# Kernel optimization log

Measured on AMD Instinct MI355X. Metric: run time of the kernel, lower is better.

Reference implementation:

```python
import jax, jax.numpy as jnp
import numpy as np
from jax.ops import segment_sum, segment_max

N, F, H, HEADS, E, OUT = 50000, 256, 64, 4, 800000, 16


def setup_inputs() -> dict:
    key = jax.random.key(0)
    ks = jax.random.split(key, 16)
    s = 0.05
    return {
        "x": jax.random.normal(ks[0], (N, F), jnp.float32),
        "edge_index": jax.random.randint(ks[1], (2, E), 0, N, jnp.int64),
        # GCN layer params
        "W_gcn1": jax.random.normal(ks[2], (F, H), jnp.float32) * s,
        "b_gcn1": jnp.zeros((H,), jnp.float32),
        "W_gcn2": jax.random.normal(ks[3], (H, OUT), jnp.float32) * s,
        "b_gcn2": jnp.zeros((OUT,), jnp.float32),
        # GAT layer 1 (heads=HEADS, concat)
        "W_gat1": jax.random.normal(ks[4], (F, HEADS * H), jnp.float32) * s,
        "a_src1": jax.random.normal(ks[5], (HEADS, H), jnp.float32) * s,
        "a_dst1": jax.random.normal(ks[6], (HEADS, H), jnp.float32) * s,
        "b_gat1": jnp.zeros((HEADS * H,), jnp.float32),
        # GAT layer 2 (heads=1, concat=False)
        "W_gat2": jax.random.normal(ks[7], (HEADS * H, OUT), jnp.float32) * s,
        "a_src2": jax.random.normal(ks[8], (1, OUT), jnp.float32) * s,
        "a_dst2": jax.random.normal(ks[9], (1, OUT), jnp.float32) * s,
        "b_gat2": jnp.zeros((OUT,), jnp.float32),
    }


def _add_self_loops(edge_index, n):
    loop = jnp.arange(n, dtype=edge_index.dtype)
    src = jnp.concatenate([edge_index[0], loop])
    dst = jnp.concatenate([edge_index[1], loop])
    return src, dst


def _gcn(x, src, dst, norm, W, b, n):
    h = x @ W  # [N, out]
    out = segment_sum(h[src] * norm[:, None], dst, num_segments=n)
    return out + b


def _gat(x, src, dst, W, a_s, a_d, b, heads, concat, n):
    h = (x @ W).reshape(n, heads, -1)  # [N, heads, C]
    s_src = jnp.einsum("nhc,hc->nh", h, a_s)
    s_dst = jnp.einsum("nhc,hc->nh", h, a_d)
    e = jax.nn.leaky_relu(s_src[src] + s_dst[dst], 0.2)  # [Etot, heads]
    m = segment_max(e, dst, num_segments=n)               # per-dst softmax
    p = jnp.exp(e - m[dst])
    denom = segment_sum(p, dst, num_segments=n)
    alpha = p / denom[dst]
    out = segment_sum(h[src] * alpha[..., None], dst, num_segments=n)
    out = out.reshape(n, -1) if concat else out.mean(axis=1)
    return out + b


def reference(x, edge_index, W_gcn1, b_gcn1, W_gcn2, b_gcn2,
              W_gat1, a_src1, a_dst1, b_gat1,
              W_gat2, a_src2, a_dst2, b_gat2):
    n = x.shape[0]
    src, dst = _add_self_loops(edge_index, n)
    # symmetric GCN normalization on self-loop-augmented graph
    deg = segment_sum(jnp.ones_like(dst, x.dtype), dst, num_segments=n)
    dinv = jnp.where(deg > 0, jax.lax.rsqrt(deg), 0.0)
    norm = dinv[src] * dinv[dst]

    x_gcn = jax.nn.relu(_gcn(x, src, dst, norm, W_gcn1, b_gcn1, n))
    x_gcn = _gcn(x_gcn, src, dst, norm, W_gcn2, b_gcn2, n)

    x_gat = jax.nn.relu(_gat(x, src, dst, W_gat1, a_src1, a_dst1, b_gat1, HEADS, True, n))
    x_gat = _gat(x_gat, src, dst, W_gat2, a_src2, a_dst2, b_gat2, 1, False, n)

    return jnp.concatenate([x_gcn, x_gat], axis=1)
```

## Files before the change

### kernel.cpp

```cpp
#include <hip/hip_runtime.h>
#include <math.h>

#define NN     50000
#define FF     256
#define HH     64
#define NHEADS 4
#define EE     800000
#define OUTD   16

typedef __attribute__((ext_vector_type(8))) short short8;
typedef __attribute__((ext_vector_type(4))) float f32x4;

__device__ inline unsigned short f2bf(float f) {
    unsigned u = __builtin_bit_cast(unsigned, f);
    unsigned r = (u + 0x7fff + ((u >> 16) & 1)) >> 16;
    return (unsigned short)r;
}
__device__ inline float bf2f(unsigned short s) {
    unsigned u = ((unsigned)s) << 16;
    return __builtin_bit_cast(float, u);
}

__global__ void k_zero_int(int* __restrict__ p, int n) {
    int i = blockIdx.x * blockDim.x + threadIdx.x;
    if (i < n) p[i] = 0;
}

__global__ void k_count(const int* __restrict__ dst, int* __restrict__ cnt, int e) {
    int i = blockIdx.x * blockDim.x + threadIdx.x;
    if (i < e) atomicAdd(&cnt[dst[i]], 1);
}

__global__ __launch_bounds__(256) void k_scan_a(const int* __restrict__ cnt,
                                                int* __restrict__ partial, int n) {
    int i = blockIdx.x * 256 + threadIdx.x;
    int v = (i < n) ? cnt[i] : 0;
#pragma unroll
    for (int off = 32; off >= 1; off >>= 1) v += __shfl_xor(v, off, 64);
    __shared__ int ws[4];
    int wave = threadIdx.x >> 6;
    if ((threadIdx.x & 63) == 0) ws[wave] = v;
    __syncthreads();
    if (threadIdx.x == 0) partial[blockIdx.x] = ws[0] + ws[1] + ws[2] + ws[3];
}

__global__ __launch_bounds__(256) void k_scan_b(const int* __restrict__ partial,
                                                int* __restrict__ blockoff,
                                                int* __restrict__ total_out, int nb) {
    __shared__ int arr[256];
    int tid = threadIdx.x;
    arr[tid] = (tid < nb) ? partial[tid] : 0;
    __syncthreads();
#pragma unroll
    for (int off = 1; off < 256; off <<= 1) {
        int v = arr[tid];
        int add = (tid >= off) ? arr[tid - off] : 0;
        __syncthreads();
        arr[tid] = v + add;
        __syncthreads();
    }
    if (tid < nb) blockoff[tid] = arr[tid] - partial[tid];
    if (tid == 0) *total_out = arr[255];
}

__global__ __launch_bounds__(256) void k_scan_c(const int* __restrict__ cnt,
                                                const int* __restrict__ blockoff,
                                                int* __restrict__ row_start,
                                                int* __restrict__ cursor,
                                                float* __restrict__ dinv, int n) {
    __shared__ int arr[256];
    int tid = threadIdx.x;
    int i = blockIdx.x * 256 + tid;
    int c = (i < n) ? cnt[i] : 0;
    arr[tid] = c;
    __syncthreads();
#pragma unroll
    for (int off = 1; off < 256; off <<= 1) {
        int v = arr[tid];
        int add = (tid >= off) ? arr[tid - off] : 0;
        __syncthreads();
        arr[tid] = v + add;
        __syncthreads();
    }
    if (i < n) {
        int excl = arr[tid] - c + blockoff[blockIdx.x];
        row_start[i] = excl;
        cursor[i] = excl;
        dinv[i] = rsqrtf((float)(c + 1));
    }
}

__global__ void k_fill(const int* __restrict__ src, const int* __restrict__ dst,
                       int* __restrict__ cursor, int* __restrict__ col, int e) {
    int i = blockIdx.x * blockDim.x + threadIdx.x;
    if (i < e) {
        int d = dst[i];
        int pos = atomicAdd(&cursor[d], 1);
        col[pos] = src[i];
    }
}

__device__ inline void pack_one(const float* __restrict__ W,
                                unsigned short* __restrict__ bhi,
                                unsigned short* __restrict__ blo,
                                int t_, int NT, int NTOT, int TOFF, int SRC_NC) {
    int lane = t_ & 63;
    int tile = (t_ >> 6) % NT;
    int kb = (t_ >> 6) / NT;
    int q = lane >> 4, c = lane & 15;
    size_t off = ((size_t)(kb * NTOT + TOFF + tile) * 64 + lane) * 8;
#pragma unroll
    for (int j = 0; j < 8; j++) {
        float w = W[(size_t)(kb * 32 + q * 8 + j) * SRC_NC + tile * 16 + c];
        unsigned short h = f2bf(w);
        bhi[off + j] = h;
        if (blo) blo[off + j] = f2bf(w - bf2f(h));
    }
}

#define NTT 20
__global__ __launch_bounds__(256) void k_pack_all(const float* __restrict__ Wg1,
                                                  const float* __restrict__ Wgat1,
                                                  const float* __restrict__ Wg2,
                                                  const float* __restrict__ Wgat2,
                                                  unsigned short* __restrict__ bhiC,
                                                  unsigned short* __restrict__ bhiG2,
                                                  unsigned short* __restrict__ bloG2,
                                                  unsigned short* __restrict__ bhiA2,
                                                  unsigned short* __restrict__ bloA2) {
    int t = blockIdx.x * 256 + threadIdx.x;
    if (t < 2048)        pack_one(Wg1,   bhiC,  nullptr, t,         4,  NTT, 0, 64);
    else if (t < 10240)  pack_one(Wgat1, bhiC,  nullptr, t - 2048,  16, NTT, 4, 256);
    else if (t < 10368)  pack_one(Wg2,   bhiG2, bloG2,   t - 10240, 1,  1,   0, 16);
    else if (t < 10880)  pack_one(Wgat2, bhiA2, bloA2,   t - 10368, 1,  1,   0, 16);
}

__global__ __launch_bounds__(256) void mfma_gemm_fused(const float* __restrict__ A,
                                                       const unsigned short* __restrict__ Bhi,
                                                       unsigned short* __restrict__ Ch1,
                                                       unsigned short* __restrict__ Chg,
                                                       const float* __restrict__ dinv,
                                                       const float* __restrict__ a_s,
                                                       const float* __restrict__ a_d,
                                                       float* __restrict__ ssrc,
                                                       float* __restrict__ sdst,
                                                       int M) {
    const int K = 256;
    __shared__ short8 bsh[NTT * 64];
    int tid = threadIdx.x;
    int w = tid >> 6, lane = tid & 63, q = lane >> 4, c = lane & 15;
    int row_base = blockIdx.x * 64 + w * 16;
    int ar = min(row_base + c, M - 1);
    const float* ap = A + (size_t)ar * K + q * 8;

    f32x4 acc[NTT];
#pragma unroll
    for (int t = 0; t < NTT; t++) acc[t] = (f32x4){0.f, 0.f, 0.f, 0.f};

    for (int kb = 0; kb < 8; kb++) {
        float av[8];
        *(float4*)(av)     = *(const float4*)(ap + kb * 32);
        *(float4*)(av + 4) = *(const float4*)(ap + kb * 32 + 4);
        short8 ahi, alo;
#pragma unroll
        for (int j = 0; j < 8; j++) {
            unsigned short h = f2bf(av[j]);
            ahi[j] = (short)h;
            alo[j] = (short)f2bf(av[j] - bf2f(h));
        }
        const short8* gh = (const short8*)(Bhi + (size_t)kb * NTT * 512);
        __syncthreads();
        for (int i = tid; i < NTT * 64; i += 256) bsh[i] = gh[i];
        __syncthreads();
#pragma unroll
        for (int t = 0; t < NTT; t++) {
            short8 bhi = bsh[t * 64 + lane];
            acc[t] = __builtin_amdgcn_mfma_f32_16x16x32_bf16(ahi, bhi, acc[t], 0, 0, 0);
            acc[t] = __builtin_amdgcn_mfma_f32_16x16x32_bf16(alo, bhi, acc[t], 0, 0, 0);
        }
    }

#pragma unroll
    for (int i = 0; i < 4; i++) {
        int r = row_base + q * 4 + i;
        float ss[4] = {0.f, 0.f, 0.f, 0.f};
        float sd[4] = {0.f, 0.f, 0.f, 0.f};
#pragma unroll
        for (int t = 0; t < 16; t++) {
            float v = acc[t + 4][i];
            ss[t >> 2] += v * a_s[t * 16 + c];
            sd[t >> 2] += v * a_d[t * 16 + c];
        }
#pragma unroll
        for (int h = 0; h < 4; h++) {
#pragma unroll
            for (int off = 1; off <= 8; off <<= 1) {
                ss[h] += __shfl_xor(ss[h], off, 16);
                sd[h] += __shfl_xor(sd[h], off, 16);
            }
        }
        if (c == i && r < M) {
            *(float4*)(ssrc + (size_t)r * 4) = make_float4(ss[0], ss[1], ss[2], ss[3]);
            *(float4*)(sdst + (size_t)r * 4) = make_float4(sd[0], sd[1], sd[2], sd[3]);
        }
    }

#pragma unroll
    for (int i = 0; i < 4; i++) {
        int r = row_base + q * 4 + i;
        if (r < M) {
            float sc = dinv[r];
#pragma unroll
            for (int t = 0; t < 4; t++)
                Ch1[(size_t)r * 64 + t * 16 + c] = f2bf(acc[t][i] * sc);
#pragma unroll
            for (int t = 0; t < 16; t++)
                Chg[(size_t)r * 256 + t * 16 + c] = f2bf(acc[t + 4][i]);
        }
    }
}

template <int KB, bool SCALE, bool SC2, int OFS>
__global__ __launch_bounds__(256) void mfma_n16(const unsigned short* __restrict__ A,
                                                const unsigned short* __restrict__ Bhi,
                                                const unsigned short* __restrict__ Blo,
                                                unsigned short* __restrict__ Cbf,
                                                const float* __restrict__ rowscale,
                                                const float* __restrict__ a_s2,
                                                const float* __restrict__ a_d2,
                                                float* __restrict__ s2s,
                                                float* __restrict__ s2d, int M) {
    const int K = KB * 32;
    int tid = threadIdx.x;
    int w = tid >> 6, lane = tid & 63, q = lane >> 4, c = lane & 15;
    int row_base = blockIdx.x * 64 + w * 16;
    int ar = min(row_base + c, M - 1);
    const unsigned short* ap = A + (size_t)ar * K + q * 8;
    f32x4 acc = (f32x4){0.f, 0.f, 0.f, 0.f};
#pragma unroll
    for (int kb = 0; kb < KB; kb++) {
        short8 av = *(const short8*)(ap + kb * 32);
        size_t bo = ((size_t)kb * 64 + lane) * 8;
        short8 bh = *(const short8*)(Bhi + bo);
        short8 bl = *(const short8*)(Blo + bo);
        acc = __builtin_amdgcn_mfma_f32_16x16x32_bf16(av, bh, acc, 0, 0, 0);
        acc = __builtin_amdgcn_mfma_f32_16x16x32_bf16(av, bl, acc, 0, 0, 0);
    }
    if (SC2) {
#pragma unroll
        for (int i = 0; i < 4; i++) {
            float ps = acc[i] * a_s2[c];
            float pd = acc[i] * a_d2[c];
#pragma unroll
            for (int off = 1; off <= 8; off <<= 1) {
                ps += __shfl_xor(ps, off, 16);
                pd += __shfl_xor(pd, off, 16);
            }
            int r = row_base + q * 4 + i;
            if (c == i && r < M) {
                s2s[r] = ps;
                s2d[r] = pd;
            }
        }
    }
#pragma unroll
    for (int i = 0; i < 4; i++) {
        int r = row_base + q * 4 + i;
        if (r < M) {
            float sc = SCALE ? rowscale[r] : 1.0f;
            Cbf[((size_t)r * 16 + c) * 2 + OFS] = f2bf(acc[i] * sc);
        }
    }
}

__global__ __launch_bounds__(256) void gcn1_agg(const unsigned short* __restrict__ h,
                                                const int* __restrict__ rs,
                                                const int* __restrict__ col,
                                                const float* __restrict__ dinv,
                                                const float* __restrict__ b,
                                                unsigned short* __restrict__ out) {
    int wid = (blockIdx.x * 256 + threadIdx.x) >> 6;
    int lane = threadIdx.x & 63;
    if (wid >= NN) return;
    int g = lane >> 4;
    int cidx = (lane & 15) * 4;
    float di = dinv[wid];
    int beg = rs[wid], end = rs[wid + 1];
    float4 acc = make_float4(0.f, 0.f, 0.f, 0.f);

    for (int j0 = beg; j0 < end; j0 += 64) {
        int cnt = min(64, end - j0);
        int sreg = 0;
        if (lane < cnt) sreg = col[j0 + lane];
        for (int e = 0; e < cnt; e += 16) {
            int m0 = e + g, m1 = e + g + 4, m2 = e + g + 8, m3 = e + g + 12;
            int s0 = __shfl(sreg, m0, 64);
            int s1 = __shfl(sreg, m1, 64);
            int s2 = __shfl(sreg, m2, 64);
            int s3 = __shfl(sreg, m3, 64);
            ushort4 v0 = make_ushort4(0, 0, 0, 0), v1 = make_ushort4(0, 0, 0, 0);
            ushort4 v2 = make_ushort4(0, 0, 0, 0), v3 = make_ushort4(0, 0, 0, 0);
            if (m0 < cnt) v0 = *(const ushort4*)(h + (size_t)s0 * HH + cidx);
            if (m1 < cnt) v1 = *(const ushort4*)(h + (size_t)s1 * HH + cidx);
            if (m2 < cnt) v2 = *(const ushort4*)(h + (size_t)s2 * HH + cidx);
            if (m3 < cnt) v3 = *(const ushort4*)(h + (size_t)s3 * HH + cidx);
            acc.x += (bf2f(v0.x) + bf2f(v1.x)) + (bf2f(v2.x) + bf2f(v3.x));
            acc.y += (bf2f(v0.y) + bf2f(v1.y)) + (bf2f(v2.y) + bf2f(v3.y));
            acc.z += (bf2f(v0.z) + bf2f(v1.z)) + (bf2f(v2.z) + bf2f(v3.z));
            acc.w += (bf2f(v0.w) + bf2f(v1.w)) + (bf2f(v2.w) + bf2f(v3.w));
        }
    }
#pragma unroll
    for (int off = 16; off <= 32; off <<= 1) {
        acc.x += __shfl_xor(acc.x, off, 64);
        acc.y += __shfl_xor(acc.y, off, 64);
        acc.z += __shfl_xor(acc.z, off, 64);
        acc.w += __shfl_xor(acc.w, off, 64);
    }
    if (g == 0) {
        ushort4 sv = *(const ushort4*)(h + (size_t)wid * HH + cidx);
        float4 bv = *(const float4*)(b + cidx);
        ushort4 o;
        o.x = f2bf(fmaxf((acc.x + bf2f(sv.x)) * di + bv.x, 0.f));
        o.y = f2bf(fmaxf((acc.y + bf2f(sv.y)) * di + bv.y, 0.f));
        o.z = f2bf(fmaxf((acc.z + bf2f(sv.z)) * di + bv.z, 0.f));
        o.w = f2bf(fmaxf((acc.w + bf2f(sv.w)) * di + bv.w, 0.f));
        *(ushort4*)(out + (size_t)wid * HH + cidx) = o;
    }
}

__global__ __launch_bounds__(256) void gat1_agg(const unsigned short* __restrict__ hg,
                                                const int* __restrict__ rs,
                                                const int* __restrict__ col,
                                                const float* __restrict__ ssrc,
                                                const float* __restrict__ sdst,
                                                const float* __restrict__ b,
                                                unsigned short* __restrict__ out) {
    __shared__ int s_lds[4][64];
    __shared__ float p_lds[4][64 * 4];
    int tid = threadIdx.x;
    int w = tid >> 6, lane = tid & 63;
    int wid = blockIdx.x * 4 + w;
    int hh = lane >> 4;
    int* sl = s_lds[w];
    float* pl = p_lds[w];

    float4 sd4 = *(const float4*)(sdst + (size_t)wid * 4);
    float sdv[4] = {sd4.x, sd4.y, sd4.z, sd4.w};
    float4 sf4 = *(const float4*)(ssrc + (size_t)wid * 4);
    float sfv[4] = {sf4.x, sf4.y, sf4.z, sf4.w};
    float psf[4];
#pragma unroll
    for (int h = 0; h < 4; h++) {
        float e = sfv[h] + sdv[h];
        e = (e >= 0.f) ? e : 0.2f * e;
        psf[h] = __expf(e);
    }
    float pse = (hh & 2) ? ((hh & 1) ? psf[3] : psf[2]) : ((hh & 1) ? psf[1] : psf[0]);
    const unsigned short* hbase = hg + lane * 4;
    ushort4 hvs = *(const ushort4*)(hbase + (size_t)wid * 256);
    float4 acc;
    acc.x = bf2f(hvs.x) * pse; acc.y = bf2f(hvs.y) * pse;
    acc.z = bf2f(hvs.z) * pse; acc.w = bf2f(hvs.w) * pse;

    float lsum[4] = {0.f, 0.f, 0.f, 0.f};
    int beg = rs[wid], end = rs[wid + 1];
    for (int j0 = beg; j0 < end; j0 += 64) {
        int cnt = min(64, end - j0);
        if (lane < cnt) {
            int sreg = col[j0 + lane];
            float4 sv = *(const float4*)(ssrc + (size_t)sreg * 4);
            float svv[4] = {sv.x, sv.y, sv.z, sv.w};
            float pv[4];
#pragma unroll
            for (int h = 0; h < 4; h++) {
                float e = svv[h] + sdv[h];
                e = (e >= 0.f) ? e : 0.2f * e;
                pv[h] = __expf(e);
                lsum[h] += pv[h];
            }
            sl[lane] = sreg;
            *(float4*)&pl[lane * 4] = make_float4(pv[0], pv[1], pv[2], pv[3]);
        }
        int e = 0;
        for (; e + 4 <= cnt; e += 4) {
            int s0 = sl[e], s1 = sl[e + 1], s2 = sl[e + 2], s3 = sl[e + 3];
            float p0 = pl[e * 4 + hh], p1 = pl[(e + 1) * 4 + hh];
            float p2 = pl[(e + 2) * 4 + hh], p3 = pl[(e + 3) * 4 + hh];
            ushort4 h0 = *(const ushort4*)(hbase + (size_t)s0 * 256);
            ushort4 h1 = *(const ushort4*)(hbase + (size_t)s1 * 256);
            ushort4 h2 = *(const ushort4*)(hbase + (size_t)s2 * 256);
            ushort4 h3 = *(const ushort4*)(hbase + (size_t)s3 * 256);
            acc.x += bf2f(h0.x) * p0; acc.y += bf2f(h0.y) * p0;
            acc.z += bf2f(h0.z) * p0; acc.w += bf2f(h0.w) * p0;
            acc.x += bf2f(h1.x) * p1; acc.y += bf2f(h1.y) * p1;
            acc.z += bf2f(h1.z) * p1; acc.w += bf2f(h1.w) * p1;
            acc.x += bf2f(h2.x) * p2; acc.y += bf2f(h2.y) * p2;
            acc.z += bf2f(h2.z) * p2; acc.w += bf2f(h2.w) * p2;
            acc.x += bf2f(h3.x) * p3; acc.y += bf2f(h3.y) * p3;
            acc.z += bf2f(h3.z) * p3; acc.w += bf2f(h3.w) * p3;
        }
        for (; e < cnt; e++) {
            int s = sl[e];
            float p = pl[e * 4 + hh];
            ushort4 hv = *(const ushort4*)(hbase + (size_t)s * 256);
            acc.x += bf2f(hv.x) * p; acc.y += bf2f(hv.y) * p;
            acc.z += bf2f(hv.z) * p; acc.w += bf2f(hv.w) * p;
        }
    }
#pragma unroll
    for (int h = 0; h < 4; h++) {
        float v = lsum[h];
        for (int off = 32; off >= 1; off >>= 1) v += __shfl_xor(v, off, 64);
        lsum[h] = v + psf[h];
    }
    float lt = (hh & 2) ? ((hh & 1) ? lsum[3] : lsum[2]) : ((hh & 1) ? lsum[1] : lsum[0]);
    float li = 1.0f / lt;
    float4 bv = *(const float4*)(b + lane * 4);
    ushort4 o;
    o.x = f2bf(fmaxf(acc.x * li + bv.x, 0.f));
    o.y = f2bf(fmaxf(acc.y * li + bv.y, 0.f));
    o.z = f2bf(fmaxf(acc.z * li + bv.z, 0.f));
    o.w = f2bf(fmaxf(acc.w * li + bv.w, 0.f));
    *(ushort4*)(out + (size_t)wid * 256 + lane * 4) = o;
}

__global__ __launch_bounds__(256) void final_agg(const unsigned* __restrict__ hp,
                                                 const int* __restrict__ rs,
                                                 const int* __restrict__ col,
                                                 const float* __restrict__ dinv,
                                                 const float* __restrict__ s2s,
                                                 const float* __restrict__ s2d,
                                                 const float* __restrict__ bg2,
                                                 const float* __restrict__ bga2,
                                                 float* __restrict__ out) {
    int t = blockIdx.x * 256 + threadIdx.x;
    int node = t >> 4;
    int c = t & 15;
    float di = dinv[node];
    float sd = s2d[node];
    float es = s2s[node] + sd;
    es = (es >= 0.f) ? es : 0.2f * es;
    float psf = __expf(es);
    unsigned pvs = hp[(size_t)node * 16 + c];
    float accg = bf2f((unsigned short)pvs);
    float acca = bf2f((unsigned short)(pvs >> 16)) * psf;
    float lp = 0.f;
    int beg = rs[node], end = rs[node + 1];
    for (int j0 = beg; j0 < end; j0 += 16) {
        int cnt = min(16, end - j0);
        int sreg = 0;
        float pr = 0.f;
        if (c < cnt) {
            sreg = col[j0 + c];
            float e = s2s[sreg] + sd;
            e = (e >= 0.f) ? e : 0.2f * e;
            pr = __expf(e);
            lp += pr;
        }
        for (int e = 0; e < cnt; e += 4) {
            int si[4];
            float pi[4];
#pragma unroll
            for (int u = 0; u < 4; u++) {
                si[u] = __shfl(sreg, (e + u) & 15, 16);
                pi[u] = __shfl(pr, (e + u) & 15, 16);
            }
            unsigned hv[4];
#pragma unroll
            for (int u = 0; u < 4; u++) hv[u] = hp[(size_t)si[u] * 16 + c];
#pragma unroll
            for (int u = 0; u < 4; u++) {
                if (e + u < cnt) {
                    accg += bf2f((unsigned short)hv[u]);
                    acca += bf2f((unsigned short)(hv[u] >> 16)) * pi[u];
                }
            }
        }
    }
    for (int off = 8; off >= 1; off >>= 1) lp += __shfl_xor(lp, off, 16);
    float l = lp + psf;
    out[(size_t)node * 32 + c] = accg * di + bg2[c];
    out[(size_t)node * 32 + 16 + c] = acca / l + bga2[c];
}

extern "C" void kernel_launch(void* const* d_in, const int* in_sizes, int n_in,
                              void* d_out, int out_size, void* d_ws, size_t ws_size,
                              hipStream_t stream) {
    const float* x      = (const float*)d_in[0];
    const int*   ei     = (const int*)d_in[1];
    const float* Wg1    = (const float*)d_in[2];
    const float* bg1    = (const float*)d_in[3];
    const float* Wg2    = (const float*)d_in[4];
    const float* bg2    = (const float*)d_in[5];
    const float* Wgat1  = (const float*)d_in[6];
    const float* a_src1 = (const float*)d_in[7];
    const float* a_dst1 = (const float*)d_in[8];
    const float* bgat1  = (const float*)d_in[9];
    const float* Wgat2  = (const float*)d_in[10];
    const float* a_src2 = (const float*)d_in[11];
    const float* a_dst2 = (const float*)d_in[12];
    const float* bgat2  = (const float*)d_in[13];
    float* out = (float*)d_out;

    const int* e_src = ei;
    const int* e_dst = ei + EE;

    char* wsb = (char*)d_ws;
    size_t o = 0;
    auto alloc = [&](size_t bytes) -> void* {
        void* p = wsb + o;
        o += (bytes + 255) & ~(size_t)255;
        return p;
    };
    float* dinv            = (float*)alloc(NN * 4);
    float* ssrc1           = (float*)alloc((size_t)NN * 16);
    float* sdst1           = (float*)alloc((size_t)NN * 16);
    unsigned short* h1b    = (unsigned short*)alloc((size_t)NN * HH * 2);
    unsigned short* xg1    = (unsigned short*)alloc((size_t)NN * HH * 2);
    unsigned short* hgb    = (unsigned short*)alloc((size_t)NN * 256 * 2);
    unsigned short* xgat1  = (unsigned short*)alloc((size_t)NN * 256 * 2);
    unsigned short* pairb  = (unsigned short*)alloc((size_t)NN * 16 * 4);
    float* s2src           = (float*)alloc(NN * 4);
    float* s2dst           = (float*)alloc(NN * 4);
    unsigned short* bhiC   = (unsigned short*)alloc((size_t)8 * NTT * 512 * 2);
    unsigned short* bhiG2  = (unsigned short*)alloc(64 * 16 * 2);
    unsigned short* bloG2  = (unsigned short*)alloc(64 * 16 * 2);
    unsigned short* bhiA2  = (unsigned short*)alloc(256 * 16 * 2);
    unsigned short* bloA2  = (unsigned short*)alloc(256 * 16 * 2);
    int* cnt               = (int*)alloc(NN * 4);
    int* rowstart          = (int*)alloc((NN + 1) * 4);
    int* cursor            = (int*)alloc(NN * 4);
    int* colarr            = (int*)alloc((size_t)EE * 4);
    int* partial           = (int*)alloc(256 * 4);
    int* blockoff          = (int*)alloc(256 * 4);

    const int TB = 256;
    const int NB = (NN + 255) / 256;
    k_zero_int<<<(NN + TB - 1) / TB, TB, 0, stream>>>(cnt, NN);
    k_count<<<(EE + TB - 1) / TB, TB, 0, stream>>>(e_dst, cnt, EE);
    k_scan_a<<<NB, TB, 0, stream>>>(cnt, partial, NN);
    k_scan_b<<<1, TB, 0, stream>>>(partial, blockoff, rowstart + NN, NB);
    k_scan_c<<<NB, TB, 0, stream>>>(cnt, blockoff, rowstart, cursor, dinv, NN);
    k_fill<<<(EE + TB - 1) / TB, TB, 0, stream>>>(e_src, e_dst, cursor, colarr, EE);
    k_pack_all<<<(10880 + TB - 1) / TB, TB, 0, stream>>>(Wg1, Wgat1, Wg2, Wgat2,
                                                         bhiC, bhiG2, bloG2,
                                                         bhiA2, bloA2);

    const int GB = (NN + 63) / 64;
    const int G16 = (NN * 16) / 256;

    mfma_gemm_fused<<<GB, TB, 0, stream>>>(x, bhiC, h1b, hgb, dinv,
                                           a_src1, a_dst1, ssrc1, sdst1, NN);

    gcn1_agg<<<(NN * 64) / TB, TB, 0, stream>>>(h1b, rowstart, colarr, dinv, bg1, xg1);
    mfma_n16<2, true, false, 0><<<GB, TB, 0, stream>>>(xg1, bhiG2, bloG2, pairb, dinv,
                                                       nullptr, nullptr, nullptr, nullptr, NN);

    gat1_agg<<<NN / 4, TB, 0, stream>>>(hgb, rowstart, colarr, ssrc1, sdst1, bgat1, xgat1);
    mfma_n16<8, false, true, 1><<<GB, TB, 0, stream>>>(xgat1, bhiA2, bloA2, pairb, nullptr,
                                                       a_src2, a_dst2, s2src, s2dst, NN);

    final_agg<<<G16, TB, 0, stream>>>((const unsigned*)pairb, rowstart, colarr, dinv,
                                      s2src, s2dst, bg2, bgat2, out);
}
```

Before: 358.1 us.

## Fuse GCN and GAT aggregations, merge second-layer GEMMs, drop LDS staging

Merges the GCN layer-1 aggregation into the GAT layer-1 aggregation kernel so both read the CSR neighbor list once and share the staged source indices. Combines the two small N=16 MFMA GEMMs into one launch by splitting blocks between them. Also removes the LDS staging and barriers for B in the first GEMM, reading B fragments directly from global/cache instead. This cuts kernel launches, repeated index reads and sync overhead, but adds register pressure in the fused aggregation and more global loads of B in the big GEMM.

```diff
diff --git a/kernel.cpp b/kernel.cpp
--- a/kernel.cpp
+++ b/kernel.cpp
@@ -146,12 +146,12 @@
                                                        float* __restrict__ sdst,
                                                        int M) {
     const int K = 256;
-    __shared__ short8 bsh[NTT * 64];
     int tid = threadIdx.x;
     int w = tid >> 6, lane = tid & 63, q = lane >> 4, c = lane & 15;
     int row_base = blockIdx.x * 64 + w * 16;
     int ar = min(row_base + c, M - 1);
     const float* ap = A + (size_t)ar * K + q * 8;
+    const short8* bp = (const short8*)Bhi + lane;
 
     f32x4 acc[NTT];
 #pragma unroll
@@ -168,13 +168,9 @@
             ahi[j] = (short)h;
             alo[j] = (short)f2bf(av[j] - bf2f(h));
         }
-        const short8* gh = (const short8*)(Bhi + (size_t)kb * NTT * 512);
-        __syncthreads();
-        for (int i = tid; i < NTT * 64; i += 256) bsh[i] = gh[i];
-        __syncthreads();
 #pragma unroll
         for (int t = 0; t < NTT; t++) {
-            short8 bhi = bsh[t * 64 + lane];
+            short8 bhi = bp[(size_t)(kb * NTT + t) * 64];
             acc[t] = __builtin_amdgcn_mfma_f32_16x16x32_bf16(ahi, bhi, acc[t], 0, 0, 0);
             acc[t] = __builtin_amdgcn_mfma_f32_16x16x32_bf16(alo, bhi, acc[t], 0, 0, 0);
         }
@@ -221,19 +217,19 @@
 }
 
 template <int KB, bool SCALE, bool SC2, int OFS>
-__global__ __launch_bounds__(256) void mfma_n16(const unsigned short* __restrict__ A,
-                                                const unsigned short* __restrict__ Bhi,
-                                                const unsigned short* __restrict__ Blo,
-                                                unsigned short* __restrict__ Cbf,
-                                                const float* __restrict__ rowscale,
-                                                const float* __restrict__ a_s2,
-                                                const float* __restrict__ a_d2,
-                                                float* __restrict__ s2s,
-                                                float* __restrict__ s2d, int M) {
+__device__ inline void n16_body(int bx, int tid,
+                                const unsigned short* __restrict__ A,
+                                const unsigned short* __restrict__ Bhi,
+                                const unsigned short* __restrict__ Blo,
+                                unsigned short* __restrict__ Cbf,
+                                const float* __restrict__ rowscale,
+                                const float* __restrict__ a_s2,
+                                const float* __restrict__ a_d2,
+                                float* __restrict__ s2s,
+                                float* __restrict__ s2d, int M) {
     const int K = KB * 32;
-    int tid = threadIdx.x;
     int w = tid >> 6, lane = tid & 63, q = lane >> 4, c = lane & 15;
-    int row_base = blockIdx.x * 64 + w * 16;
+    int row_base = bx * 64 + w * 16;
     int ar = min(row_base + c, M - 1);
     const unsigned short* ap = A + (size_t)ar * K + q * 8;
     f32x4 acc = (f32x4){0.f, 0.f, 0.f, 0.f};
@@ -273,78 +269,50 @@
     }
 }
 
-__global__ __launch_bounds__(256) void gcn1_agg(const unsigned short* __restrict__ h,
-                                                const int* __restrict__ rs,
-                                                const int* __restrict__ col,
-                                                const float* __restrict__ dinv,
-                                                const float* __restrict__ b,
-                                                unsigned short* __restrict__ out) {
-    int wid = (blockIdx.x * 256 + threadIdx.x) >> 6;
-    int lane = threadIdx.x & 63;
-    if (wid >= NN) return;
-    int g = lane >> 4;
-    int cidx = (lane & 15) * 4;
-    float di = dinv[wid];
-    int beg = rs[wid], end = rs[wid + 1];
-    float4 acc = make_float4(0.f, 0.f, 0.f, 0.f);
-
-    for (int j0 = beg; j0 < end; j0 += 64) {
-        int cnt = min(64, end - j0);
-        int sreg = 0;
-        if (lane < cnt) sreg = col[j0 + lane];
-        for (int e = 0; e < cnt; e += 16) {
-            int m0 = e + g, m1 = e + g + 4, m2 = e + g + 8, m3 = e + g + 12;
-            int s0 = __shfl(sreg, m0, 64);
-            int s1 = __shfl(sreg, m1, 64);
-            int s2 = __shfl(sreg, m2, 64);
-            int s3 = __shfl(sreg, m3, 64);
-            ushort4 v0 = make_ushort4(0, 0, 0, 0), v1 = make_ushort4(0, 0, 0, 0);
-            ushort4 v2 = make_ushort4(0, 0, 0, 0), v3 = make_ushort4(0, 0, 0, 0);
-            if (m0 < cnt) v0 = *(const ushort4*)(h + (size_t)s0 * HH + cidx);
-            if (m1 < cnt) v1 = *(const ushort4*)(h + (size_t)s1 * HH + cidx);
-            if (m2 < cnt) v2 = *(const ushort4*)(h + (size_t)s2 * HH + cidx);
-            if (m3 < cnt) v3 = *(const ushort4*)(h + (size_t)s3 * HH + cidx);
-            acc.x += (bf2f(v0.x) + bf2f(v1.x)) + (bf2f(v2.x) + bf2f(v3.x));
-            acc.y += (bf2f(v0.y) + bf2f(v1.y)) + (bf2f(v2.y) + bf2f(v3.y));
-            acc.z += (bf2f(v0.z) + bf2f(v1.z)) + (bf2f(v2.z) + bf2f(v3.z));
-            acc.w += (bf2f(v0.w) + bf2f(v1.w)) + (bf2f(v2.w) + bf2f(v3.w));
-        }
-    }
-#pragma unroll
-    for (int off = 16; off <= 32; off <<= 1) {
-        acc.x += __shfl_xor(acc.x, off, 64);
-        acc.y += __shfl_xor(acc.y, off, 64);
-        acc.z += __shfl_xor(acc.z, off, 64);
-        acc.w += __shfl_xor(acc.w, off, 64);
-    }
-    if (g == 0) {
-        ushort4 sv = *(const ushort4*)(h + (size_t)wid * HH + cidx);
-        float4 bv = *(const float4*)(b + cidx);
-        ushort4 o;
-        o.x = f2bf(fmaxf((acc.x + bf2f(sv.x)) * di + bv.x, 0.f));
-        o.y = f2bf(fmaxf((acc.y + bf2f(sv.y)) * di + bv.y, 0.f));
-        o.z = f2bf(fmaxf((acc.z + bf2f(sv.z)) * di + bv.z, 0.f));
-        o.w = f2bf(fmaxf((acc.w + bf2f(sv.w)) * di + bv.w, 0.f));
-        *(ushort4*)(out + (size_t)wid * HH + cidx) = o;
-    }
-}
-
-__global__ __launch_bounds__(256) void gat1_agg(const unsigned short* __restrict__ hg,
+__global__ __launch_bounds__(256) void mfma_n16_both(const unsigned short* __restrict__ Ag,
+                                                     const unsigned short* __restrict__ Ac,
+                                                     const unsigned short* __restrict__ bhiA2,
+                                                     const unsigned short* __restrict__ bloA2,
+                                                     const unsigned short* __restrict__ bhiG2,
+                                                     const unsigned short* __restrict__ bloG2,
+                                                     unsigned short* __restrict__ pairb,
+                                                     const float* __restrict__ dinv,
+                                                     const float* __restrict__ a_s2,
+                                                     const float* __restrict__ a_d2,
+                                                     float* __restrict__ s2s,
+                                                     float* __restrict__ s2d,
+                                                     int M, int GB) {
+    int bx = blockIdx.x;
+    if (bx < GB)
+        n16_body<8, false, true, 1>(bx, threadIdx.x, Ag, bhiA2, bloA2, pairb,
+                                    nullptr, a_s2, a_d2, s2s, s2d, M);
+    else
+        n16_body<2, true, false, 0>(bx - GB, threadIdx.x, Ac, bhiG2, bloG2, pairb,
+                                    dinv, nullptr, nullptr, nullptr, nullptr, M);
+}
+
+__global__ __launch_bounds__(256) void both_agg(const unsigned short* __restrict__ hg,
+                                                const unsigned short* __restrict__ h1,
                                                 const int* __restrict__ rs,
                                                 const int* __restrict__ col,
                                                 const float* __restrict__ ssrc,
                                                 const float* __restrict__ sdst,
-                                                const float* __restrict__ b,
-                                                unsigned short* __restrict__ out) {
+                                                const float* __restrict__ dinv,
+                                                const float* __restrict__ bgat,
+                                                const float* __restrict__ bgcn,
+                                                unsigned short* __restrict__ outg,
+                                                unsigned short* __restrict__ outc) {
     __shared__ int s_lds[4][64];
     __shared__ float p_lds[4][64 * 4];
     int tid = threadIdx.x;
     int w = tid >> 6, lane = tid & 63;
     int wid = blockIdx.x * 4 + w;
     int hh = lane >> 4;
+    int cidx = (lane & 15) * 4;
     int* sl = s_lds[w];
     float* pl = p_lds[w];
 
+    float di = dinv[wid];
     float4 sd4 = *(const float4*)(sdst + (size_t)wid * 4);
     float sdv[4] = {sd4.x, sd4.y, sd4.z, sd4.w};
     float4 sf4 = *(const float4*)(ssrc + (size_t)wid * 4);
@@ -362,6 +330,7 @@
     float4 acc;
     acc.x = bf2f(hvs.x) * pse; acc.y = bf2f(hvs.y) * pse;
     acc.z = bf2f(hvs.z) * pse; acc.w = bf2f(hvs.w) * pse;
+    float4 accc = make_float4(0.f, 0.f, 0.f, 0.f);
 
     float lsum[4] = {0.f, 0.f, 0.f, 0.f};
     int beg = rs[wid], end = rs[wid + 1];
@@ -388,13 +357,13 @@
             float p0 = pl[e * 4 + hh], p1 = pl[(e + 1) * 4 + hh];
             float p2 = pl[(e + 2) * 4 + hh], p3 = pl[(e + 3) * 4 + hh];
             ushort4 h0 = *(const ushort4*)(hbase + (size_t)s0 * 256);
-            ushort4 h1 = *(const ushort4*)(hbase + (size_t)s1 * 256);
+            ushort4 h1v = *(const ushort4*)(hbase + (size_t)s1 * 256);
             ushort4 h2 = *(const ushort4*)(hbase + (size_t)s2 * 256);
             ushort4 h3 = *(const ushort4*)(hbase + (size_t)s3 * 256);
             acc.x += bf2f(h0.x) * p0; acc.y += bf2f(h0.y) * p0;
             acc.z += bf2f(h0.z) * p0; acc.w += bf2f(h0.w) * p0;
-            acc.x += bf2f(h1.x) * p1; acc.y += bf2f(h1.y) * p1;
-            acc.z += bf2f(h1.z) * p1; acc.w += bf2f(h1.w) * p1;
+            acc.x += bf2f(h1v.x) * p1; acc.y += bf2f(h1v.y) * p1;
+            acc.z += bf2f(h1v.z) * p1; acc.w += bf2f(h1v.w) * p1;
             acc.x += bf2f(h2.x) * p2; acc.y += bf2f(h2.y) * p2;
             acc.z += bf2f(h2.z) * p2; acc.w += bf2f(h2.w) * p2;
             acc.x += bf2f(h3.x) * p3; acc.y += bf2f(h3.y) * p3;
@@ -407,6 +376,22 @@
             acc.x += bf2f(hv.x) * p; acc.y += bf2f(hv.y) * p;
             acc.z += bf2f(hv.z) * p; acc.w += bf2f(hv.w) * p;
         }
+        int e2 = hh;
+        for (; e2 + 4 < cnt; e2 += 8) {
+            int sa = sl[e2], sb = sl[e2 + 4];
+            ushort4 va = *(const ushort4*)(h1 + (size_t)sa * HH + cidx);
+            ushort4 vb = *(const ushort4*)(h1 + (size_t)sb * HH + cidx);
+            accc.x += bf2f(va.x) + bf2f(vb.x);
+            accc.y += bf2f(va.y) + bf2f(vb.y);
+            accc.z += bf2f(va.z) + bf2f(vb.z);
+            accc.w += bf2f(va.w) + bf2f(vb.w);
+        }
+        if (e2 < cnt) {
+            int sa = sl[e2];
+            ushort4 va = *(const ushort4*)(h1 + (size_t)sa * HH + cidx);
+            accc.x += bf2f(va.x); accc.y += bf2f(va.y);
+            accc.z += bf2f(va.z); accc.w += bf2f(va.w);
+        }
     }
 #pragma unroll
     for (int h = 0; h < 4; h++) {
@@ -416,13 +401,30 @@
     }
     float lt = (hh & 2) ? ((hh & 1) ? lsum[3] : lsum[2]) : ((hh & 1) ? lsum[1] : lsum[0]);
     float li = 1.0f / lt;
-    float4 bv = *(const float4*)(b + lane * 4);
+    float4 bv = *(const float4*)(bgat + lane * 4);
     ushort4 o;
     o.x = f2bf(fmaxf(acc.x * li + bv.x, 0.f));
     o.y = f2bf(fmaxf(acc.y * li + bv.y, 0.f));
     o.z = f2bf(fmaxf(acc.z * li + bv.z, 0.f));
     o.w = f2bf(fmaxf(acc.w * li + bv.w, 0.f));
-    *(ushort4*)(out + (size_t)wid * 256 + lane * 4) = o;
+    *(ushort4*)(outg + (size_t)wid * 256 + lane * 4) = o;
+#pragma unroll
+    for (int off = 16; off <= 32; off <<= 1) {
+        accc.x += __shfl_xor(accc.x, off, 64);
+        accc.y += __shfl_xor(accc.y, off, 64);
+        accc.z += __shfl_xor(accc.z, off, 64);
+        accc.w += __shfl_xor(accc.w, off, 64);
+    }
+    if (hh == 0) {
+        ushort4 sv = *(const ushort4*)(h1 + (size_t)wid * HH + cidx);
+        float4 bc = *(const float4*)(bgcn + cidx);
+        ushort4 oc;
+        oc.x = f2bf(fmaxf((accc.x + bf2f(sv.x)) * di + bc.x, 0.f));
+        oc.y = f2bf(fmaxf((accc.y + bf2f(sv.y)) * di + bc.y, 0.f));
+        oc.z = f2bf(fmaxf((accc.z + bf2f(sv.z)) * di + bc.z, 0.f));
+        oc.w = f2bf(fmaxf((accc.w + bf2f(sv.w)) * di + bc.w, 0.f));
+        *(ushort4*)(outc + (size_t)wid * HH + cidx) = oc;
+    }
 }
 
 __global__ __launch_bounds__(256) void final_agg(const unsigned* __restrict__ hp,
@@ -553,13 +555,12 @@
     mfma_gemm_fused<<<GB, TB, 0, stream>>>(x, bhiC, h1b, hgb, dinv,
                                            a_src1, a_dst1, ssrc1, sdst1, NN);
 
-    gcn1_agg<<<(NN * 64) / TB, TB, 0, stream>>>(h1b, rowstart, colarr, dinv, bg1, xg1);
-    mfma_n16<2, true, false, 0><<<GB, TB, 0, stream>>>(xg1, bhiG2, bloG2, pairb, dinv,
-                                                       nullptr, nullptr, nullptr, nullptr, NN);
-
-    gat1_agg<<<NN / 4, TB, 0, stream>>>(hgb, rowstart, colarr, ssrc1, sdst1, bgat1, xgat1);
-    mfma_n16<8, false, true, 1><<<GB, TB, 0, stream>>>(xgat1, bhiA2, bloA2, pairb, nullptr,
-                                                       a_src2, a_dst2, s2src, s2dst, NN);
+    both_agg<<<NN / 4, TB, 0, stream>>>(hgb, h1b, rowstart, colarr, ssrc1, sdst1,
+                                        dinv, bgat1, bg1, xgat1, xg1);
+
+    mfma_n16_both<<<2 * GB, TB, 0, stream>>>(xgat1, xg1, bhiA2, bloA2, bhiG2, bloG2,
+                                             pairb, dinv, a_src2, a_dst2,
+                                             s2src, s2dst, NN, GB);
 
     final_agg<<<G16, TB, 0, stream>>>((const unsigned*)pairb, rowstart, colarr, dinv,
                                       s2src, s2dst, bg2, bgat2, out);
```

After: 355.2 us. No clear change (-0.8%).
